# Kernel optimization log

Hardware: AMD Instinct MI355X
Metric: run time of the kernel (lower is better)

Reference implementation:

```python
import jax, jax.numpy as jnp
import numpy as np

N = 50000   # num nodes
E = 400000  # num edges (avg degree 8)
D = 256     # in_channels
H = 256     # hidden_channels
C = 64      # out_channels
K = 2       # k_hops


def setup_inputs() -> dict:
    key = jax.random.key(0)
    ks = jax.random.split(key, 10)
    x = jax.random.normal(ks[0], (N, D), dtype=jnp.float32)
    edge_index = jax.random.randint(ks[1], (2, E), 0, N, dtype=jnp.int32)
    s = 0.05
    # per-hop linears of the single H2GCNConv (weights stored [in, out])
    W0 = jax.random.normal(ks[2], (D, H), jnp.float32) * s
    W1 = jax.random.normal(ks[3], (D, H), jnp.float32) * s
    W2 = jax.random.normal(ks[4], (D, H), jnp.float32) * s
    b0 = jnp.zeros((H,), jnp.float32)
    b1 = jnp.zeros((H,), jnp.float32)
    b2 = jnp.zeros((H,), jnp.float32)
    # classifier: h2_out_dim = H*(K+1) = 768 -> C
    Wc = jax.random.normal(ks[5], (H * (K + 1), C), jnp.float32) * s
    bc = jnp.zeros((C,), jnp.float32)
    return {"x": x, "edge_index": edge_index, "num_nodes": N,
            "W0": W0, "b0": b0, "W1": W1, "b1": b1, "W2": W2, "b2": b2,
            "Wc": Wc, "bc": bc}


def _normalize_adj(edge_index, num_nodes):
    # add self loops, then D^{-1/2} A D^{-1/2} edge weights
    loops = jnp.arange(num_nodes, dtype=edge_index.dtype)
    ei = jnp.concatenate([edge_index, jnp.stack([loops, loops])], axis=1)
    row, col = ei[0], ei[1]
    deg = jax.ops.segment_sum(jnp.ones(row.shape[0], jnp.float32), row,
                              num_segments=num_nodes)
    dis = jnp.where(deg > 0, deg ** -0.5, 0.0)  # inf -> 0 for isolated nodes
    return ei, dis[row] * dis[col]


def _sparse_mm(edge_index, edge_weight, x, num_nodes):
    # gather -> scale -> scatter-add (COO SpMM)
    row, col = edge_index[0], edge_index[1]
    msg = x[col] * edge_weight[:, None]  # [E', F]
    return jax.ops.segment_sum(msg, row, num_segments=num_nodes)


def reference(x, edge_index, num_nodes, W0, b0, W1, b1, W2, b2, Wc, bc):
    ei, ew = _normalize_adj(edge_index, num_nodes)
    # H2GCNConv: ego + k-hop aggregates, each through its own linear, concat
    outs = [x @ W0 + b0]
    cur = x
    for Wk, bk in ((W1, b1), (W2, b2)):
        cur = _sparse_mm(ei, ew, cur, num_nodes)
        outs.append(cur @ Wk + bk)
    h = jax.nn.relu(jnp.concatenate(outs, axis=1))  # [N, 3H]
    # dropout p=0 / eval mode -> identity
    return h @ Wc + bc
```

## Files before the change

### kernel.cpp

```cpp
#include <hip/hip_runtime.h>


#define FD 256
#define CO 64
#define SB 512
#define MT1 391
#define PS (50048 * 256)

using frag_ab = __attribute__((ext_vector_type(8))) short;
using f32x4   = __attribute__((ext_vector_type(4))) float;
typedef unsigned short u16;
typedef unsigned int   u32;

__device__ __forceinline__ u16 f2bf(float f) {
    u32 u = __builtin_bit_cast(u32, f);
    return (u16)((u + 0x7FFFu + ((u >> 16) & 1u)) >> 16);
}
__device__ __forceinline__ float bf2f(u16 u) {
    u32 v = ((u32)u) << 16;
    return __builtin_bit_cast(float, v);
}
__device__ __forceinline__ float bfl(u32 packed) {
    return __builtin_bit_cast(float, packed << 16);
}
__device__ __forceinline__ float bfh(u32 packed) {
    return __builtin_bit_cast(float, packed & 0xFFFF0000u);
}

__device__ __forceinline__ void gll16(const void* g, void* l) {
    __builtin_amdgcn_global_load_lds(
        (const __attribute__((address_space(1))) u32*)g,
        (__attribute__((address_space(3))) u32*)l, 16, 0, 0);
}

#define BAR()  __builtin_amdgcn_s_barrier()
#define WLG0() asm volatile("s_waitcnt lgkmcnt(0)" ::: "memory")
#define WVM0() asm volatile("s_waitcnt vmcnt(0)" ::: "memory")
#define WVM2() asm volatile("s_waitcnt vmcnt(2)" ::: "memory")

__global__ void init_kernel(int* deg, int* fill, int n) {
    int i = blockIdx.x * blockDim.x + threadIdx.x;
    if (i < n) { deg[i] = 1; fill[i] = 0; }
}
__global__ void count_kernel(const int* __restrict__ ei0, int* deg, int e) {
    int i = blockIdx.x * blockDim.x + threadIdx.x;
    if (i < e) atomicAdd(&deg[ei0[i]], 1);
}
__global__ void scan1(const int* __restrict__ deg, int* __restrict__ rowptr,
                      int* __restrict__ bsum, float* __restrict__ dis, int n) {
    __shared__ int sh[SB];
    int tid = threadIdx.x;
    int i = blockIdx.x * SB + tid;
    int v = (i < n) ? deg[i] : 0;
    if (i < n) dis[i] = rsqrtf((float)v);
    sh[tid] = v;
    __syncthreads();
    for (int off = 1; off < SB; off <<= 1) {
        int add = (tid >= off) ? sh[tid - off] : 0;
        __syncthreads();
        sh[tid] += add;
        __syncthreads();
    }
    if (i < n) rowptr[i] = sh[tid] - v;
    if (tid == SB - 1) bsum[blockIdx.x] = sh[tid];
}
__global__ void scan2(const int* __restrict__ bsum, int* __restrict__ bscan, int nb) {
    __shared__ int sh[128];
    int tid = threadIdx.x;
    int v = (tid < nb) ? bsum[tid] : 0;
    sh[tid] = v;
    __syncthreads();
    for (int off = 1; off < 128; off <<= 1) {
        int add = (tid >= off) ? sh[tid - off] : 0;
        __syncthreads();
        sh[tid] += add;
        __syncthreads();
    }
    if (tid < nb) bscan[tid] = sh[tid] - v;
    if (tid == nb - 1) bscan[nb] = sh[tid];
}
__global__ void scan3(int* rowptr, const int* __restrict__ bscan, int n, int nb) {
    int i = blockIdx.x * 256 + threadIdx.x;
    if (i < n) rowptr[i] += bscan[i / SB];
    if (i == n) rowptr[n] = bscan[nb];
}
__global__ void fill_kernel(const int* __restrict__ ei, const float* __restrict__ dis,
                            const int* __restrict__ rowptr, int* fill,
                            int* __restrict__ col, float* __restrict__ wv, int e, int n) {
    int i = blockIdx.x * blockDim.x + threadIdx.x;
    if (i >= e + n) return;
    int r, c;
    if (i < e) { r = ei[i]; c = ei[e + i]; }
    else       { r = i - e; c = r; }
    float w = dis[r] * dis[c];
    int pos = rowptr[r] + atomicAdd(&fill[r], 1);
    col[pos] = c;
    wv[pos]  = w;
}

__global__ void conv_kernel(const float* __restrict__ x, u16* __restrict__ xb, int total4) {
    int i = blockIdx.x * blockDim.x + threadIdx.x;
    if (i < total4) {
        float4 v = ((const float4*)x)[i];
        ushort4 o;
        o.x = f2bf(v.x); o.y = f2bf(v.y); o.z = f2bf(v.z); o.w = f2bf(v.w);
        ((ushort4*)xb)[i] = o;
    }
}
__global__ void wtrans_kernel(const float* __restrict__ W0, const float* __restrict__ W1,
                              const float* __restrict__ W2, const float* __restrict__ Wc,
                              u16* __restrict__ WkT, u16* __restrict__ WcT) {
    __shared__ u16 tl[64][65];
    int b = blockIdx.x;
    const float* src; u16* dst; int R, C, r0, c0;
    if (b < 48) {
        int k = b >> 4, t = b & 15;
        src = (k == 0) ? W0 : (k == 1) ? W1 : W2;
        dst = WkT + k * 65536;
        R = 256; C = 256; r0 = (t >> 2) * 64; c0 = (t & 3) * 64;
    } else {
        int t = b - 48;
        src = Wc; dst = WcT;
        R = 768; C = 64; r0 = t * 64; c0 = 0;
    }
    int tid = threadIdx.x;
    int rr = tid >> 4, cc = (tid & 15) * 4;
    #pragma unroll
    for (int it = 0; it < 4; ++it) {
        int r = it * 16 + rr;
        float4 v = *(const float4*)(src + (size_t)(r0 + r) * C + c0 + cc);
        tl[cc + 0][r] = f2bf(v.x); tl[cc + 1][r] = f2bf(v.y);
        tl[cc + 2][r] = f2bf(v.z); tl[cc + 3][r] = f2bf(v.w);
    }
    __syncthreads();
    #pragma unroll
    for (int it = 0; it < 4; ++it) {
        int crow = it * 16 + rr;
        ushort4 o;
        o.x = tl[crow][cc + 0]; o.y = tl[crow][cc + 1];
        o.z = tl[crow][cc + 2]; o.w = tl[crow][cc + 3];
        *(ushort4*)(dst + (size_t)(c0 + crow) * R + r0 + cc) = o;
    }
}

__global__ void spmm_bf16(const int* __restrict__ rowptr, const int* __restrict__ col,
                          const float* __restrict__ wv, const u16* __restrict__ xb,
                          u16* __restrict__ outb, int n) {
    int tid = threadIdx.x;
    int lane = tid & 63;
    int row = blockIdx.x * 8 + ((tid >> 6) << 1) + (lane >> 5);
    if (row >= n) return;
    int l32 = lane & 31;
    int p0 = rowptr[row], p1 = rowptr[row + 1];
    float a[8];
    #pragma unroll
    for (int j = 0; j < 8; ++j) a[j] = 0.f;

    int p = p0;
    for (; p + 8 <= p1; p += 8) {
        int c[8]; float wt[8]; uint4 v[8];
        #pragma unroll
        for (int u = 0; u < 8; ++u) { c[u] = col[p + u]; wt[u] = wv[p + u]; }
        #pragma unroll
        for (int u = 0; u < 8; ++u)
            v[u] = *(const uint4*)(xb + (size_t)c[u] * FD + l32 * 8);
        #pragma unroll
        for (int u = 0; u < 8; ++u) {
            a[0] += wt[u] * bfl(v[u].x); a[1] += wt[u] * bfh(v[u].x);
            a[2] += wt[u] * bfl(v[u].y); a[3] += wt[u] * bfh(v[u].y);
            a[4] += wt[u] * bfl(v[u].z); a[5] += wt[u] * bfh(v[u].z);
            a[6] += wt[u] * bfl(v[u].w); a[7] += wt[u] * bfh(v[u].w);
        }
    }
    for (; p + 2 <= p1; p += 2) {
        int c[2]; float wt[2]; uint4 v[2];
        #pragma unroll
        for (int u = 0; u < 2; ++u) { c[u] = col[p + u]; wt[u] = wv[p + u]; }
        #pragma unroll
        for (int u = 0; u < 2; ++u)
            v[u] = *(const uint4*)(xb + (size_t)c[u] * FD + l32 * 8);
        #pragma unroll
        for (int u = 0; u < 2; ++u) {
            a[0] += wt[u] * bfl(v[u].x); a[1] += wt[u] * bfh(v[u].x);
            a[2] += wt[u] * bfl(v[u].y); a[3] += wt[u] * bfh(v[u].y);
            a[4] += wt[u] * bfl(v[u].z); a[5] += wt[u] * bfh(v[u].z);
            a[6] += wt[u] * bfl(v[u].w); a[7] += wt[u] * bfh(v[u].w);
        }
    }
    for (; p < p1; ++p) {
        int c = col[p];
        float wt = wv[p];
        uint4 v = *(const uint4*)(xb + (size_t)c * FD + l32 * 8);
        a[0] += wt * bfl(v.x); a[1] += wt * bfh(v.x);
        a[2] += wt * bfl(v.y); a[3] += wt * bfh(v.y);
        a[4] += wt * bfl(v.z); a[5] += wt * bfh(v.z);
        a[6] += wt * bfl(v.w); a[7] += wt * bfh(v.w);
    }
    uint4 o;
    o.x = (u32)f2bf(a[0]) | ((u32)f2bf(a[1]) << 16);
    o.y = (u32)f2bf(a[2]) | ((u32)f2bf(a[3]) << 16);
    o.z = (u32)f2bf(a[4]) | ((u32)f2bf(a[5]) << 16);
    o.w = (u32)f2bf(a[6]) | ((u32)f2bf(a[7]) << 16);
    *(uint4*)(outb + (size_t)row * FD + l32 * 8) = o;
}

__launch_bounds__(256, 3)
__global__ void gemm1(const u16* __restrict__ xb, const u16* __restrict__ agg1b,
                      const u16* __restrict__ agg2b, const u16* __restrict__ WkT,
                      const float* __restrict__ b0, const float* __restrict__ b1,
                      const float* __restrict__ b2, u16* __restrict__ T, int n) {
    __shared__ __align__(16) char lds[32768];
    char* lA = lds;
    char* lB = lds + 16384;

    const int tid = threadIdx.x;
    const int w = tid >> 6, l = tid & 63;
    const int l4 = l >> 4, lm = l & 15;
    const int mq = w & 1, nq = w >> 1;

    int bid = blockIdx.x;
    const int nt  = bid & 1;
    int rest = bid >> 1;
    const int mt  = rest % MT1;
    const int seg = rest / MT1;
    const int row0 = mt * 128;
    const int n0   = nt * 128;

    const u16* inb = (seg == 0) ? xb : (seg == 1) ? agg1b : agg2b;
    const u16* WT  = WkT + (size_t)seg * 65536;
    const float* bk = (seg == 0) ? b0 : (seg == 1) ? b1 : b2;

    f32x4 acc[4][4];
    #pragma unroll
    for (int jm = 0; jm < 4; ++jm)
        #pragma unroll
        for (int rn = 0; rn < 4; ++rn) acc[jm][rn] = (f32x4)(0.f);

    for (int kt = 0; kt < 4; ++kt) {
        WLG0();
        BAR();
        #pragma unroll
        for (int c = 0; c < 4; ++c) {
            int L = w * 1024 + c * 4096 + l * 16;
            int r = L >> 7, s = (L >> 4) & 7;
            int k16 = s ^ (r & 7);
            int gr = row0 + r; if (gr > n - 1) gr = n - 1;
            gll16(inb + (size_t)gr * FD + kt * 64 + k16 * 8, lA + w * 1024 + c * 4096);
        }
        #pragma unroll
        for (int c = 0; c < 4; ++c) {
            int L = w * 1024 + c * 4096 + l * 16;
            int r = L >> 7, s = (L >> 4) & 7;
            int k16 = s ^ (r & 7);
            gll16(WT + (size_t)(n0 + r) * FD + kt * 64 + k16 * 8, lB + w * 1024 + c * 4096);
        }
        WVM0();
        BAR();

        #pragma unroll
        for (int kk2 = 0; kk2 < 2; ++kk2) {
            frag_ab af[4], bf_[4];
            #pragma unroll
            for (int jm = 0; jm < 4; ++jm) {
                int rB = nq * 64 + jm * 16 + lm;
                af[jm] = *(const frag_ab*)(lB + rB * 128 + (((kk2 * 4 + l4) ^ (rB & 7)) << 4));
            }
            #pragma unroll
            for (int rn = 0; rn < 4; ++rn) {
                int rA = mq * 64 + rn * 16 + lm;
                bf_[rn] = *(const frag_ab*)(lA + rA * 128 + (((kk2 * 4 + l4) ^ (rA & 7)) << 4));
            }
            #pragma unroll
            for (int jm = 0; jm < 4; ++jm)
                #pragma unroll
                for (int rn = 0; rn < 4; ++rn)
                    acc[jm][rn] = __builtin_amdgcn_mfma_f32_16x16x32_bf16(af[jm], bf_[rn], acc[jm][rn], 0, 0, 0);
        }
    }

    u16* Tp = T + (size_t)seg * PS;
    #pragma unroll
    for (int jm = 0; jm < 4; ++jm) {
        int j = n0 + nq * 64 + jm * 16 + l4 * 4;
        float4 bb = *(const float4*)(bk + j);
        #pragma unroll
        for (int rn = 0; rn < 4; ++rn) {
            int r = row0 + mq * 64 + rn * 16 + lm;
            f32x4 v = acc[jm][rn];
            ushort4 p;
            p.x = f2bf(fmaxf(v[0] + bb.x, 0.f));
            p.y = f2bf(fmaxf(v[1] + bb.y, 0.f));
            p.z = f2bf(fmaxf(v[2] + bb.z, 0.f));
            p.w = f2bf(fmaxf(v[3] + bb.w, 0.f));
            *(ushort4*)(Tp + (size_t)r * FD + j) = p;
        }
    }
}

__launch_bounds__(256, 3)
__global__ void gemm2(const u16* __restrict__ T, const u16* __restrict__ WcT,
                      const float* __restrict__ bc, float* __restrict__ out, int n) {
    __shared__ __align__(16) char lds[16384];
    const int tid = threadIdx.x;
    const int w = tid >> 6, l = tid & 63;
    const int l4 = l >> 4, lm = l & 15;
    const int row0 = blockIdx.x * 64;
    const int rr = w * 16 + lm;
    const int r  = row0 + rr;

    frag_ab b[24];
    #pragma unroll
    for (int kt = 0; kt < 12; ++kt)
        #pragma unroll
        for (int kk2 = 0; kk2 < 2; ++kk2)
            b[kt * 2 + kk2] = *(const frag_ab*)(T + (size_t)(kt >> 2) * PS +
                                                (size_t)r * FD + (kt & 3) * 64 + kk2 * 32 + l4 * 8);

    auto stageW = [&](int kt, char* buf) {
        #pragma unroll
        for (int i = 0; i < 2; ++i) {
            int L = tid * 16 + i * 4096;
            int c = L >> 7, s = (L >> 4) & 7;
            gll16(WcT + (size_t)c * 768 + kt * 64 + (s ^ (c & 7)) * 8,
                  buf + w * 1024 + i * 4096);
        }
    };

    f32x4 acc[4];
    #pragma unroll
    for (int am = 0; am < 4; ++am) acc[am] = (f32x4)(0.f);

    stageW(0, lds);
    #pragma unroll
    for (int kt = 0; kt < 12; ++kt) {
        char* cur = lds + (kt & 1) * 8192;
        if (kt < 11) {
            stageW(kt + 1, lds + ((kt + 1) & 1) * 8192);
            WVM2();
        } else {
            WVM0();
        }
        BAR();
        #pragma unroll
        for (int kk2 = 0; kk2 < 2; ++kk2) {
            #pragma unroll
            for (int am = 0; am < 4; ++am) {
                int c = am * 16 + lm;
                frag_ab afr = *(const frag_ab*)(cur + c * 128 + (((kk2 * 4 + l4) ^ (c & 7)) << 4));
                acc[am] = __builtin_amdgcn_mfma_f32_16x16x32_bf16(afr, b[kt * 2 + kk2], acc[am], 0, 0, 0);
            }
        }
        WLG0();
        BAR();
    }

    if (r < n) {
        #pragma unroll
        for (int am = 0; am < 4; ++am) {
            float4 bb = *(const float4*)(bc + am * 16 + l4 * 4);
            float4 o;
            o.x = acc[am][0] + bb.x;
            o.y = acc[am][1] + bb.y;
            o.z = acc[am][2] + bb.z;
            o.w = acc[am][3] + bb.w;
            *(float4*)(out + (size_t)r * CO + am * 16 + l4 * 4) = o;
        }
    }
}

extern "C" void kernel_launch(void* const* d_in, const int* in_sizes, int n_in,
                              void* d_out, int out_size, void* d_ws, size_t ws_size,
                              hipStream_t stream) {
    const float* x  = (const float*)d_in[0];
    const int*   ei = (const int*)d_in[1];
    const float* W0 = (const float*)d_in[3];
    const float* b0 = (const float*)d_in[4];
    const float* W1 = (const float*)d_in[5];
    const float* b1 = (const float*)d_in[6];
    const float* W2 = (const float*)d_in[7];
    const float* b2 = (const float*)d_in[8];
    const float* Wc = (const float*)d_in[9];
    const float* bc = (const float*)d_in[10];
    float* out = (float*)d_out;

    const int n  = in_sizes[0] / FD;
    const int e  = in_sizes[1] / 2;
    const int ep = e + n;
    const int nb = (n + SB - 1) / SB;

    char* ws = (char*)d_ws;
    size_t o = 0;
    auto take = [&](size_t nbytes) -> char* {
        char* p = ws + o;
        o += (nbytes + 255) & ~(size_t)255;
        return p;
    };
    int*   deg    = (int*)  take((size_t)n * 4);
    int*   fill   = (int*)  take((size_t)n * 4);
    float* dis    = (float*)take((size_t)n * 4);
    int*   rowptr = (int*)  take((size_t)(n + 1) * 4);
    int*   bsum   = (int*)  take((size_t)(nb + 1) * 4);
    int*   bscan  = (int*)  take((size_t)(nb + 1) * 4);
    int*   col    = (int*)  take((size_t)ep * 4);
    float* wv     = (float*)take((size_t)ep * 4);
    u16*   xb     = (u16*)  take((size_t)n * FD * 2);
    u16*   agg1b  = (u16*)  take((size_t)n * FD * 2);
    u16*   agg2b  = (u16*)  take((size_t)n * FD * 2);
    u16*   WkT    = (u16*)  take((size_t)3 * FD * FD * 2);
    u16*   WcT    = (u16*)  take((size_t)CO * 3 * FD * 2);
    u16*   T      = (u16*)  take((size_t)3 * PS * 2);
    (void)ws_size; (void)n_in; (void)out_size;

    init_kernel <<<(n + 255) / 256, 256, 0, stream>>>(deg, fill, n);
    count_kernel<<<(e + 255) / 256, 256, 0, stream>>>(ei, deg, e);
    scan1       <<<nb, SB, 0, stream>>>(deg, rowptr, bsum, dis, n);
    scan2       <<<1, 128, 0, stream>>>(bsum, bscan, nb);
    scan3       <<<(n + 256) / 256, 256, 0, stream>>>(rowptr, bscan, n, nb);
    fill_kernel <<<(ep + 255) / 256, 256, 0, stream>>>(ei, dis, rowptr, fill, col, wv, e, n);

    const int total4 = n * FD / 4;
    conv_kernel  <<<(total4 + 255) / 256, 256, 0, stream>>>(x, xb, total4);
    wtrans_kernel<<<60, 256, 0, stream>>>(W0, W1, W2, Wc, WkT, WcT);

    spmm_bf16<<<(n + 7) / 8, 256, 0, stream>>>(rowptr, col, wv, xb, agg1b, n);
    spmm_bf16<<<(n + 7) / 8, 256, 0, stream>>>(rowptr, col, wv, agg1b, agg2b, n);

    gemm1<<<2 * MT1 * 3, 256, 0, stream>>>(xb, agg1b, agg2b, WkT, b0, b1, b2, T, n);
    gemm2<<<(n + 63) / 64, 256, 0, stream>>>(T, WcT, bc, out, n);
}
```

Baseline: 221.7 us.

## Double-buffer gemm1 LDS staging and pack CSR column/weight into int2

gemm1 now uses two 32KB LDS buffers so the global-to-LDS load for the next k-tile is issued before the MFMA work on the current tile, overlapping load latency with compute. In exchange it lowers the launch-bounds occupancy hint from 3 to 2 blocks per CU. Separately, the CSR column index and edge weight are stored interleaved as int2, so the SpMM fetches both with one 8-byte load instead of two separate 4-byte loads.

```diff
diff --git a/kernel.cpp b/kernel.cpp
--- a/kernel.cpp
+++ b/kernel.cpp
@@ -15,10 +15,6 @@
 __device__ __forceinline__ u16 f2bf(float f) {
     u32 u = __builtin_bit_cast(u32, f);
     return (u16)((u + 0x7FFFu + ((u >> 16) & 1u)) >> 16);
-}
-__device__ __forceinline__ float bf2f(u16 u) {
-    u32 v = ((u32)u) << 16;
-    return __builtin_bit_cast(float, v);
 }
 __device__ __forceinline__ float bfl(u32 packed) {
     return __builtin_bit_cast(float, packed << 16);
@@ -86,7 +82,7 @@
 }
 __global__ void fill_kernel(const int* __restrict__ ei, const float* __restrict__ dis,
                             const int* __restrict__ rowptr, int* fill,
-                            int* __restrict__ col, float* __restrict__ wv, int e, int n) {
+                            int2* __restrict__ cw, int e, int n) {
     int i = blockIdx.x * blockDim.x + threadIdx.x;
     if (i >= e + n) return;
     int r, c;
@@ -94,8 +90,8 @@
     else       { r = i - e; c = r; }
     float w = dis[r] * dis[c];
     int pos = rowptr[r] + atomicAdd(&fill[r], 1);
-    col[pos] = c;
-    wv[pos]  = w;
+    int2 p; p.x = c; p.y = __float_as_int(w);
+    cw[pos] = p;
 }
 
 __global__ void conv_kernel(const float* __restrict__ x, u16* __restrict__ xb, int total4) {
@@ -143,9 +139,8 @@
     }
 }
 
-__global__ void spmm_bf16(const int* __restrict__ rowptr, const int* __restrict__ col,
-                          const float* __restrict__ wv, const u16* __restrict__ xb,
-                          u16* __restrict__ outb, int n) {
+__global__ void spmm_bf16(const int* __restrict__ rowptr, const int2* __restrict__ cw,
+                          const u16* __restrict__ xb, u16* __restrict__ outb, int n) {
     int tid = threadIdx.x;
     int lane = tid & 63;
     int row = blockIdx.x * 8 + ((tid >> 6) << 1) + (lane >> 5);
@@ -158,39 +153,41 @@
 
     int p = p0;
     for (; p + 8 <= p1; p += 8) {
-        int c[8]; float wt[8]; uint4 v[8];
-        #pragma unroll
-        for (int u = 0; u < 8; ++u) { c[u] = col[p + u]; wt[u] = wv[p + u]; }
+        int2 cwv[8]; uint4 v[8];
+        #pragma unroll
+        for (int u = 0; u < 8; ++u) cwv[u] = cw[p + u];
         #pragma unroll
         for (int u = 0; u < 8; ++u)
-            v[u] = *(const uint4*)(xb + (size_t)c[u] * FD + l32 * 8);
+            v[u] = *(const uint4*)(xb + (size_t)cwv[u].x * FD + l32 * 8);
         #pragma unroll
         for (int u = 0; u < 8; ++u) {
-            a[0] += wt[u] * bfl(v[u].x); a[1] += wt[u] * bfh(v[u].x);
-            a[2] += wt[u] * bfl(v[u].y); a[3] += wt[u] * bfh(v[u].y);
-            a[4] += wt[u] * bfl(v[u].z); a[5] += wt[u] * bfh(v[u].z);
-            a[6] += wt[u] * bfl(v[u].w); a[7] += wt[u] * bfh(v[u].w);
+            float wt = __int_as_float(cwv[u].y);
+            a[0] += wt * bfl(v[u].x); a[1] += wt * bfh(v[u].x);
+            a[2] += wt * bfl(v[u].y); a[3] += wt * bfh(v[u].y);
+            a[4] += wt * bfl(v[u].z); a[5] += wt * bfh(v[u].z);
+            a[6] += wt * bfl(v[u].w); a[7] += wt * bfh(v[u].w);
         }
     }
     for (; p + 2 <= p1; p += 2) {
-        int c[2]; float wt[2]; uint4 v[2];
-        #pragma unroll
-        for (int u = 0; u < 2; ++u) { c[u] = col[p + u]; wt[u] = wv[p + u]; }
+        int2 cwv[2]; uint4 v[2];
+        #pragma unroll
+        for (int u = 0; u < 2; ++u) cwv[u] = cw[p + u];
         #pragma unroll
         for (int u = 0; u < 2; ++u)
-            v[u] = *(const uint4*)(xb + (size_t)c[u] * FD + l32 * 8);
+            v[u] = *(const uint4*)(xb + (size_t)cwv[u].x * FD + l32 * 8);
         #pragma unroll
         for (int u = 0; u < 2; ++u) {
-            a[0] += wt[u] * bfl(v[u].x); a[1] += wt[u] * bfh(v[u].x);
-            a[2] += wt[u] * bfl(v[u].y); a[3] += wt[u] * bfh(v[u].y);
-            a[4] += wt[u] * bfl(v[u].z); a[5] += wt[u] * bfh(v[u].z);
-            a[6] += wt[u] * bfl(v[u].w); a[7] += wt[u] * bfh(v[u].w);
+            float wt = __int_as_float(cwv[u].y);
+            a[0] += wt * bfl(v[u].x); a[1] += wt * bfh(v[u].x);
+            a[2] += wt * bfl(v[u].y); a[3] += wt * bfh(v[u].y);
+            a[4] += wt * bfl(v[u].z); a[5] += wt * bfh(v[u].z);
+            a[6] += wt * bfl(v[u].w); a[7] += wt * bfh(v[u].w);
         }
     }
     for (; p < p1; ++p) {
-        int c = col[p];
-        float wt = wv[p];
-        uint4 v = *(const uint4*)(xb + (size_t)c * FD + l32 * 8);
+        int2 cwv = cw[p];
+        float wt = __int_as_float(cwv.y);
+        uint4 v = *(const uint4*)(xb + (size_t)cwv.x * FD + l32 * 8);
         a[0] += wt * bfl(v.x); a[1] += wt * bfh(v.x);
         a[2] += wt * bfl(v.y); a[3] += wt * bfh(v.y);
         a[4] += wt * bfl(v.z); a[5] += wt * bfh(v.z);
@@ -204,14 +201,12 @@
     *(uint4*)(outb + (size_t)row * FD + l32 * 8) = o;
 }
 
-__launch_bounds__(256, 3)
+__launch_bounds__(256, 2)
 __global__ void gemm1(const u16* __restrict__ xb, const u16* __restrict__ agg1b,
                       const u16* __restrict__ agg2b, const u16* __restrict__ WkT,
                       const float* __restrict__ b0, const float* __restrict__ b1,
                       const float* __restrict__ b2, u16* __restrict__ T, int n) {
-    __shared__ __align__(16) char lds[32768];
-    char* lA = lds;
-    char* lB = lds + 16384;
+    __shared__ __align__(16) char lds[65536];
 
     const int tid = threadIdx.x;
     const int w = tid >> 6, l = tid & 63;
@@ -230,32 +225,39 @@
     const u16* WT  = WkT + (size_t)seg * 65536;
     const float* bk = (seg == 0) ? b0 : (seg == 1) ? b1 : b2;
 
-    f32x4 acc[4][4];
-    #pragma unroll
-    for (int jm = 0; jm < 4; ++jm)
-        #pragma unroll
-        for (int rn = 0; rn < 4; ++rn) acc[jm][rn] = (f32x4)(0.f);
-
-    for (int kt = 0; kt < 4; ++kt) {
-        WLG0();
-        BAR();
+    auto stage = [&](int kt, char* buf) {
         #pragma unroll
         for (int c = 0; c < 4; ++c) {
             int L = w * 1024 + c * 4096 + l * 16;
             int r = L >> 7, s = (L >> 4) & 7;
             int k16 = s ^ (r & 7);
             int gr = row0 + r; if (gr > n - 1) gr = n - 1;
-            gll16(inb + (size_t)gr * FD + kt * 64 + k16 * 8, lA + w * 1024 + c * 4096);
+            gll16(inb + (size_t)gr * FD + kt * 64 + k16 * 8, buf + w * 1024 + c * 4096);
         }
         #pragma unroll
         for (int c = 0; c < 4; ++c) {
             int L = w * 1024 + c * 4096 + l * 16;
             int r = L >> 7, s = (L >> 4) & 7;
             int k16 = s ^ (r & 7);
-            gll16(WT + (size_t)(n0 + r) * FD + kt * 64 + k16 * 8, lB + w * 1024 + c * 4096);
-        }
-        WVM0();
-        BAR();
+            gll16(WT + (size_t)(n0 + r) * FD + kt * 64 + k16 * 8,
+                  buf + 16384 + w * 1024 + c * 4096);
+        }
+    };
+
+    f32x4 acc[4][4];
+    #pragma unroll
+    for (int jm = 0; jm < 4; ++jm)
+        #pragma unroll
+        for (int rn = 0; rn < 4; ++rn) acc[jm][rn] = (f32x4)(0.f);
+
+    stage(0, lds);
+    WVM0();
+    BAR();
+
+    #pragma unroll
+    for (int kt = 0; kt < 4; ++kt) {
+        char* cur = lds + (kt & 1) * 32768;
+        if (kt < 3) stage(kt + 1, lds + ((kt + 1) & 1) * 32768);
 
         #pragma unroll
         for (int kk2 = 0; kk2 < 2; ++kk2) {
@@ -263,12 +265,12 @@
             #pragma unroll
             for (int jm = 0; jm < 4; ++jm) {
                 int rB = nq * 64 + jm * 16 + lm;
-                af[jm] = *(const frag_ab*)(lB + rB * 128 + (((kk2 * 4 + l4) ^ (rB & 7)) << 4));
+                af[jm] = *(const frag_ab*)(cur + 16384 + rB * 128 + (((kk2 * 4 + l4) ^ (rB & 7)) << 4));
             }
             #pragma unroll
             for (int rn = 0; rn < 4; ++rn) {
                 int rA = mq * 64 + rn * 16 + lm;
-                bf_[rn] = *(const frag_ab*)(lA + rA * 128 + (((kk2 * 4 + l4) ^ (rA & 7)) << 4));
+                bf_[rn] = *(const frag_ab*)(cur + rA * 128 + (((kk2 * 4 + l4) ^ (rA & 7)) << 4));
             }
             #pragma unroll
             for (int jm = 0; jm < 4; ++jm)
@@ -276,6 +278,10 @@
                 for (int rn = 0; rn < 4; ++rn)
                     acc[jm][rn] = __builtin_amdgcn_mfma_f32_16x16x32_bf16(af[jm], bf_[rn], acc[jm][rn], 0, 0, 0);
         }
+
+        if (kt < 3) WVM0();
+        WLG0();
+        BAR();
     }
 
     u16* Tp = T + (size_t)seg * PS;
@@ -401,8 +407,7 @@
     int*   rowptr = (int*)  take((size_t)(n + 1) * 4);
     int*   bsum   = (int*)  take((size_t)(nb + 1) * 4);
     int*   bscan  = (int*)  take((size_t)(nb + 1) * 4);
-    int*   col    = (int*)  take((size_t)ep * 4);
-    float* wv     = (float*)take((size_t)ep * 4);
+    int2*  cw     = (int2*) take((size_t)ep * 8);
     u16*   xb     = (u16*)  take((size_t)n * FD * 2);
     u16*   agg1b  = (u16*)  take((size_t)n * FD * 2);
     u16*   agg2b  = (u16*)  take((size_t)n * FD * 2);
@@ -416,14 +421,14 @@
     scan1       <<<nb, SB, 0, stream>>>(deg, rowptr, bsum, dis, n);
     scan2       <<<1, 128, 0, stream>>>(bsum, bscan, nb);
     scan3       <<<(n + 256) / 256, 256, 0, stream>>>(rowptr, bscan, n, nb);
-    fill_kernel <<<(ep + 255) / 256, 256, 0, stream>>>(ei, dis, rowptr, fill, col, wv, e, n);
+    fill_kernel <<<(ep + 255) / 256, 256, 0, stream>>>(ei, dis, rowptr, fill, cw, e, n);
 
     const int total4 = n * FD / 4;
     conv_kernel  <<<(total4 + 255) / 256, 256, 0, stream>>>(x, xb, total4);
     wtrans_kernel<<<60, 256, 0, stream>>>(W0, W1, W2, Wc, WkT, WcT);
 
-    spmm_bf16<<<(n + 7) / 8, 256, 0, stream>>>(rowptr, col, wv, xb, agg1b, n);
-    spmm_bf16<<<(n + 7) / 8, 256, 0, stream>>>(rowptr, col, wv, agg1b, agg2b, n);
+    spmm_bf16<<<(n + 7) / 8, 256, 0, stream>>>(rowptr, cw, xb, agg1b, n);
+    spmm_bf16<<<(n + 7) / 8, 256, 0, stream>>>(rowptr, cw, agg1b, agg2b, n);
 
     gemm1<<<2 * MT1 * 3, 256, 0, stream>>>(xb, agg1b, agg2b, WkT, b0, b1, b2, T, n);
     gemm2<<<(n + 63) / 64, 256, 0, stream>>>(T, WcT, bc, out, n);
```

Result: no change. 223.0 us (+0.6%).
